# Optimization experiments

Hardware: AMD Instinct MI355X
Metric: run time of the kernel (lower is better)

## Reference

```python
import jax, jax.numpy as jnp
import numpy as np
import math

NEG = -1e32
B, S, D, H, DFF, L = 16, 512, 1024, 8, 4096, 3
DK = D // H


def layernorm(x, g, b, eps=1e-5):
    mu = x.mean(-1, keepdims=True)
    var = ((x - mu) ** 2).mean(-1, keepdims=True)
    return (x - mu) / jnp.sqrt(var + eps) * g + b


def gen_dam(alphas, E, bmask):
    # alphas, E: [H, S, 2]; hard gumbel-softmax with straight-through
    Hh, Ss, _ = alphas.shape
    g = -jnp.log(E + 1e-5)
    y_soft = jax.nn.softmax(alphas + g, axis=-1)  # tau = 1
    idx = jnp.argmax(y_soft, axis=-1)
    y_hard = jax.nn.one_hot(idx, 2, dtype=y_soft.dtype)
    m = y_hard - jax.lax.stop_gradient(y_soft) + y_soft
    m = jnp.broadcast_to(m[:, :, 0:1], (Hh, Ss, Ss))
    m = jnp.triu(m)
    m = jnp.rot90(m, 1, axes=(1, 2))
    i = jnp.arange(Ss)[:, None]
    j = jnp.arange(Ss)[None, :]
    src = jnp.clip(j - i, 0, Ss - 1)
    shifted = m[:, jnp.arange(Ss)[:, None], src]  # mask_tri[:, i, j] = m[:, i, j - i]
    mask_tri = jnp.where(j >= i, shifted, 0.0)
    masks = mask_tri + jnp.swapaxes(jnp.triu(mask_tri, 1), 1, 2)
    masks = jnp.triu(masks, bmask)
    return masks


def attention(q, k, v, src_mask, dam, zero_pad, gammas):
    # q,k,v: [B,H,S,dk]; src_mask: [S,S] bool; dam: [H,S,S] bool
    dk = q.shape[-1]
    Ss = q.shape[2]
    scores = jnp.einsum('bhqd,bhkd->bhqk', q, k) / math.sqrt(dk)
    damb = dam[None]          # [1,H,S,S]
    smb = src_mask[None, None]  # [1,1,S,S]
    # NOTE: faithful to the torch code, where the first masked_fill(mask==0)
    # result is overwritten - only dam masks the first softmax.
    sc = jnp.where(damb, scores, NEG)
    sc = jax.nn.softmax(sc, axis=-1)
    sc = sc * smb.astype(sc.dtype) * damb.astype(sc.dtype)
    distcum = jnp.cumsum(sc, axis=-1)
    disttot = jnp.sum(sc, axis=-1, keepdims=True)
    pos = jnp.abs(jnp.arange(Ss)[None, :] - jnp.arange(Ss)[:, None]).astype(scores.dtype)
    dist = jnp.sqrt(jnp.clip((disttot - distcum) * pos[None, None], 0.0, None))
    dist = jax.lax.stop_gradient(dist)
    gamma = -jax.nn.softplus(gammas)[None]  # [1,H,1,1]
    te = jnp.clip(jnp.exp(dist * gamma), 1e-5, 1e5)
    scores = scores * te
    scores = jnp.where(smb, scores, NEG)
    scores = jnp.where(damb, scores, NEG)
    scores = jax.nn.softmax(scores, axis=-1)
    if zero_pad:
        scores = scores.at[:, :, 0, :].set(0.0)
    return jnp.einsum('bhqk,bhkd->bhqd', scores, v)


def transformer_layer(bmask, query, key, values, apply_pos, p):
    Bb, Ss, Dd = query.shape
    Hh = p['gammas'].shape[0]
    dam = gen_dam(p['alphas'], p['E'], bmask) == 0
    src_mask = jnp.triu(jnp.ones((Ss, Ss), jnp.int32), bmask) == 0
    k = (key @ p['kW'].T + p['kb']).reshape(Bb, Ss, Hh, -1).transpose(0, 2, 1, 3)
    q = (query @ p['kW'].T + p['kb']).reshape(Bb, Ss, Hh, -1).transpose(0, 2, 1, 3)  # kq_same
    v = (values @ p['vW'].T + p['vb']).reshape(Bb, Ss, Hh, -1).transpose(0, 2, 1, 3)
    att = attention(q, k, v, src_mask, dam, bmask == 0, p['gammas'])
    concat = att.transpose(0, 2, 1, 3).reshape(Bb, Ss, Dd)
    q2 = concat @ p['oW'].T + p['ob']
    x = layernorm(query + q2, p['ln1_g'], p['ln1_b'])
    if apply_pos:
        ff = jax.nn.relu(x @ p['w1'].T + p['b1']) @ p['w2'].T + p['b2']
        x = layernorm(x + ff, p['ln2_g'], p['ln2_b'])
    return x


def setup_inputs() -> dict:
    key = jax.random.key(0)
    ks = jax.random.split(key, 16)
    sc = 0.02
    return {
        'q_embed_data': jax.random.normal(ks[0], (B, S, D), jnp.float32),
        'qa_embed_data': jax.random.normal(ks[1], (B, S, D), jnp.float32),
        'kW': sc * jax.random.normal(ks[2], (L, D, D), jnp.float32),
        'kb': jnp.zeros((L, D), jnp.float32),
        'vW': sc * jax.random.normal(ks[3], (L, D, D), jnp.float32),
        'vb': jnp.zeros((L, D), jnp.float32),
        'oW': sc * jax.random.normal(ks[4], (L, D, D), jnp.float32),
        'ob': jnp.zeros((L, D), jnp.float32),
        'gammas': 0.5 * jax.random.normal(ks[5], (L, H, 1, 1), jnp.float32),
        'alphas': 0.001 * jax.random.normal(ks[6], (L, H, S, 2), jnp.float32),
        'ln1_g': jnp.ones((L, D), jnp.float32),
        'ln1_b': jnp.zeros((L, D), jnp.float32),
        'w1': sc * jax.random.normal(ks[7], (L, DFF, D), jnp.float32),
        'b1': jnp.zeros((L, DFF), jnp.float32),
        'w2': sc * jax.random.normal(ks[8], (L, D, DFF), jnp.float32),
        'b2': jnp.zeros((L, D), jnp.float32),
        'ln2_g': jnp.ones((L, D), jnp.float32),
        'ln2_b': jnp.zeros((L, D), jnp.float32),
        'gumbel_E': jax.random.exponential(ks[9], (L, H, S, 2), jnp.float32),
    }


def reference(q_embed_data, qa_embed_data, kW, kb, vW, vb, oW, ob, gammas,
              alphas, ln1_g, ln1_b, w1, b1, w2, b2, ln2_g, ln2_b, gumbel_E):
    def P(l):
        return {'kW': kW[l], 'kb': kb[l], 'vW': vW[l], 'vb': vb[l],
                'oW': oW[l], 'ob': ob[l], 'gammas': gammas[l], 'alphas': alphas[l],
                'ln1_g': ln1_g[l], 'ln1_b': ln1_b[l], 'w1': w1[l], 'b1': b1[l],
                'w2': w2[l], 'b2': b2[l], 'ln2_g': ln2_g[l], 'ln2_b': ln2_b[l],
                'E': gumbel_E[l]}
    # blocks_1: self-attention over answer embedding (mask=1)
    y = transformer_layer(1, qa_embed_data, qa_embed_data, qa_embed_data, True, P(0))
    # blocks_2: self-attn on question emb (no FFN), then cross-attn into y
    x = transformer_layer(1, q_embed_data, q_embed_data, q_embed_data, False, P(1))
    x = transformer_layer(0, x, x, y, True, P(2))
    return x
```

## Files before the change

### kernel.cpp

```cpp
#include <hip/hip_runtime.h>
#include <math.h>

#define NEGV -1e32f

typedef __bf16 bf16_t;
typedef _Float16 f16_t;
typedef __bf16 bf16x8 __attribute__((ext_vector_type(8)));
typedef __bf16 bf16x4 __attribute__((ext_vector_type(4)));
typedef _Float16 f16x8 __attribute__((ext_vector_type(8)));
typedef float floatx4 __attribute__((ext_vector_type(4)));

static __device__ __forceinline__ float wave_sum(float v) {
#pragma unroll
  for (int d = 32; d > 0; d >>= 1) v += __shfl_xor(v, d, 64);
  return v;
}
static __device__ __forceinline__ float wave_max(float v) {
#pragma unroll
  for (int d = 32; d > 0; d >>= 1) v = fmaxf(v, __shfl_xor(v, d, 64));
  return v;
}

static __device__ __forceinline__ void gl2lds16(const bf16_t* g, bf16_t* l) {
  __builtin_amdgcn_global_load_lds((__attribute__((address_space(1))) void*)(void*)g,
                                   (__attribute__((address_space(3))) void*)l, 16, 0, 0);
}

template <int BIAS_MODE, bool RELU, int OUT_MODE>
__global__ __launch_bounds__(256) void gemm_bt(
    const bf16_t* __restrict__ A, long lda, long a_so, long a_si,
    const bf16_t* __restrict__ B, long ldb, long b_so, long b_si,
    void* __restrict__ Cv, long ldc, long c_so, long c_si,
    const float* __restrict__ bias, int zdiv, int K, float alpha)
{
  __shared__ bf16_t As[8192];
  __shared__ bf16_t Bs[8192];
  const int tid = threadIdx.x;
  const int wave = tid >> 6;
  const int lane = tid & 63;
  const int wr = wave >> 1;
  const int wc = wave & 1;
  const int z = blockIdx.z;
  const long zo = z / zdiv;
  const long zi = z % zdiv;
  A += zo * a_so + zi * a_si;
  B += zo * b_so + zi * b_si;
  const long m0 = (long)blockIdx.x * 128;
  const long n0 = (long)blockIdx.y * 128;

  const int srow = tid >> 3;
  const int scol = ((tid & 7) ^ (srow & 7)) * 8;
  const bf16_t* gA = A + (m0 + srow) * lda + scol;
  const bf16_t* gB = B + (n0 + srow) * ldb + scol;
  bf16_t* lA = As + wave * 512;
  bf16_t* lB = Bs + wave * 512;

  floatx4 acc[4][4] = {};
  const int lr = lane & 15;
  const int kg = lane >> 4;

  for (int k0 = 0; k0 < K; k0 += 64) {
#pragma unroll
    for (int r = 0; r < 4; ++r) {
      gl2lds16(gA + (long)r * 32 * lda + k0, lA + r * 2048);
      gl2lds16(gB + (long)r * 32 * ldb + k0, lB + r * 2048);
    }
    __syncthreads();
#pragma unroll
    for (int h = 0; h < 2; ++h) {
      const int slot = ((h * 4 + kg) ^ (lr & 7)) * 8;
      bf16x8 af[4], bfr[4];
#pragma unroll
      for (int t = 0; t < 4; ++t) {
        af[t]  = *(const bf16x8*)(As + (wr * 64 + t * 16 + lr) * 64 + slot);
        bfr[t] = *(const bf16x8*)(Bs + (wc * 64 + t * 16 + lr) * 64 + slot);
      }
#pragma unroll
      for (int tm = 0; tm < 4; ++tm)
#pragma unroll
        for (int tn = 0; tn < 4; ++tn)
          acc[tm][tn] = __builtin_amdgcn_mfma_f32_16x16x32_bf16(af[tm], bfr[tn], acc[tm][tn], 0, 0, 0);
    }
    __syncthreads();
  }

  const long coff = zo * c_so + zi * c_si;
  const int q4 = (lane >> 4) * 4;
#pragma unroll
  for (int tm = 0; tm < 4; ++tm) {
#pragma unroll
    for (int tn = 0; tn < 4; ++tn) {
#pragma unroll
      for (int r = 0; r < 4; ++r) {
        const long row = m0 + wr * 64 + tm * 16 + q4 + r;
        const long col = n0 + wc * 64 + tn * 16 + lr;
        float v = acc[tm][tn][r] * alpha;
        if (BIAS_MODE == 1) v += bias[col];
        if (BIAS_MODE == 2) v += bias[row];
        if (RELU) v = fmaxf(v, 0.0f);
        const long idx = coff + row * ldc + col;
        if (OUT_MODE == 1)      ((bf16_t*)Cv)[idx] = (bf16_t)v;
        else if (OUT_MODE == 2) ((f16_t*)Cv)[idx]  = (f16_t)v;
        else                    ((float*)Cv)[idx]  = v;
      }
    }
  }
}

__global__ __launch_bounds__(256) void cast_kernel(const float* __restrict__ in,
                                                   bf16_t* __restrict__ out, long n)
{
  const long i = ((long)blockIdx.x * 256 + threadIdx.x) * 4;
  if (i >= n) return;
  const float4 v = *(const float4*)(in + i);
  bf16x4 o;
  o[0] = (bf16_t)v.x; o[1] = (bf16_t)v.y; o[2] = (bf16_t)v.z; o[3] = (bf16_t)v.w;
  *(bf16x4*)(out + i) = o;
}

__global__ void bbit_kernel(const float* __restrict__ alphas, const float* __restrict__ E,
                            int* __restrict__ bbit, int n)
{
  const int i = blockIdx.x * 256 + threadIdx.x;
  if (i >= n) return;
  const float l0 = alphas[2 * i]     - logf(E[2 * i]     + 1e-5f);
  const float l1 = alphas[2 * i + 1] - logf(E[2 * i + 1] + 1e-5f);
  bbit[i] = (l0 >= l1) ? 1 : 0;
}

template <bool XBF>
__global__ __launch_bounds__(256) void ln_kernel(
    const void* __restrict__ Xv, const float* __restrict__ R,
    const float* __restrict__ g, const float* __restrict__ b,
    float* __restrict__ out32, bf16_t* __restrict__ out16)
{
  const long row = blockIdx.x;
  const int t = threadIdx.x;
  float x0, x1, x2, x3;
  if (XBF) {
    const bf16x4 xv = *(const bf16x4*)((const bf16_t*)Xv + row * 1024 + t * 4);
    x0 = (float)xv[0]; x1 = (float)xv[1]; x2 = (float)xv[2]; x3 = (float)xv[3];
  } else {
    const float4 xv = *(const float4*)((const float*)Xv + row * 1024 + t * 4);
    x0 = xv.x; x1 = xv.y; x2 = xv.z; x3 = xv.w;
  }
  const float4 rv = *(const float4*)(R + row * 1024 + t * 4);
  const float v0 = x0 + rv.x, v1 = x1 + rv.y, v2 = x2 + rv.z, v3 = x3 + rv.w;
  float s  = v0 + v1 + v2 + v3;
  float s2 = v0 * v0 + v1 * v1 + v2 * v2 + v3 * v3;
  s = wave_sum(s); s2 = wave_sum(s2);
  __shared__ float red[8];
  const int wv = t >> 6, lane = t & 63;
  if (lane == 0) { red[wv] = s; red[4 + wv] = s2; }
  __syncthreads();
  s  = red[0] + red[1] + red[2] + red[3];
  s2 = red[4] + red[5] + red[6] + red[7];
  const float mu = s * (1.0f / 1024.0f);
  const float var = s2 * (1.0f / 1024.0f) - mu * mu;
  const float rstd = rsqrtf(var + 1e-5f);
  const float4 gv = *(const float4*)(g + t * 4);
  const float4 bv = *(const float4*)(b + t * 4);
  float4 ov;
  ov.x = (v0 - mu) * rstd * gv.x + bv.x;
  ov.y = (v1 - mu) * rstd * gv.y + bv.y;
  ov.z = (v2 - mu) * rstd * gv.z + bv.z;
  ov.w = (v3 - mu) * rstd * gv.w + bv.w;
  if (out32) *(float4*)(out32 + row * 1024 + t * 4) = ov;
  if (out16) {
    bf16x4 oh;
    oh[0] = (bf16_t)ov.x; oh[1] = (bf16_t)ov.y; oh[2] = (bf16_t)ov.z; oh[3] = (bf16_t)ov.w;
    *(bf16x4*)(out16 + row * 1024 + t * 4) = oh;
  }
}

__global__ __launch_bounds__(256) void attn_mid(
    const f16_t* __restrict__ S, bf16_t* __restrict__ P,
    const int* __restrict__ bbit, const float* __restrict__ gam,
    const int bmask, const int zero_pad)
{
  const int wid = threadIdx.x >> 6;
  const int lane = threadIdx.x & 63;
  const long rowid = (long)blockIdx.x * 4 + wid;
  const int i = (int)(rowid & 511);
  const int h = (int)(rowid >> 9) & 7;
  const f16_t* s = S + rowid * 512;
  const int jb = lane * 8;

  const float gv = gam[h];
  const float gamma = -log1pf(expf(gv));

  float sv[8];
  {
    const f16x8 a = *(const f16x8*)(s + jb);
#pragma unroll
    for (int u = 0; u < 8; ++u) sv[u] = (float)a[u];
  }
  const int* bb = bbit + h * 512;
  float z[8];
  bool band[8];
  float m1 = NEGV;
#pragma unroll
  for (int u = 0; u < 8; ++u) {
    const int j = jb + u;
    const bool bd = j < i + bmask;
    band[u] = bd;
    int d = j - i; d = d < 0 ? 0 : d;
    const bool allowed = bd || (bb[d] == 0);
    z[u] = allowed ? sv[u] : NEGV;
    m1 = fmaxf(m1, z[u]);
  }
  m1 = wave_max(m1);
  float e[8], es = 0.f;
#pragma unroll
  for (int u = 0; u < 8; ++u) { e[u] = expf(z[u] - m1); es += e[u]; }
  es = wave_sum(es);
  const float inv1 = 1.0f / es;

  float c[8];
  float run = 0.f;
#pragma unroll
  for (int u = 0; u < 8; ++u) {
    const float p = band[u] ? e[u] * inv1 : 0.f;
    run += p;
    c[u] = run;
  }
  float x = run;
#pragma unroll
  for (int d = 1; d < 64; d <<= 1) {
    const float y = __shfl_up(x, (unsigned)d, 64);
    if (lane >= d) x += y;
  }
  const float tot = __shfl(x, 63, 64);
  const float ex = x - run;

  float z2[8];
  float m2 = NEGV;
#pragma unroll
  for (int u = 0; u < 8; ++u) {
    const int j = jb + u;
    const float cc = c[u] + ex;
    const float pos = fabsf((float)(i - j));
    const float dist = sqrtf(fmaxf((tot - cc) * pos, 0.f));
    float te = expf(dist * gamma);
    te = fminf(fmaxf(te, 1e-5f), 1e5f);
    z2[u] = band[u] ? sv[u] * te : NEGV;
    m2 = fmaxf(m2, z2[u]);
  }
  m2 = wave_max(m2);
  float f[8], es2 = 0.f;
#pragma unroll
  for (int u = 0; u < 8; ++u) { f[u] = expf(z2[u] - m2); es2 += f[u]; }
  es2 = wave_sum(es2);
  const float inv2 = (zero_pad && i == 0) ? 0.f : (1.0f / es2);
  bf16x8 o;
#pragma unroll
  for (int u = 0; u < 8; ++u) o[u] = (bf16_t)(f[u] * inv2);
  *(bf16x8*)(P + rowid * 512 + jb) = o;
}

extern "C" void kernel_launch(void* const* d_in, const int* in_sizes, int n_in,
                              void* d_out, int out_size, void* d_ws, size_t ws_size,
                              hipStream_t stream)
{
  (void)in_sizes; (void)n_in; (void)out_size; (void)ws_size;
  const float* q_emb  = (const float*)d_in[0];
  const float* qa_emb = (const float*)d_in[1];
  const float* kW = (const float*)d_in[2];
  const float* kb = (const float*)d_in[3];
  const float* vW = (const float*)d_in[4];
  const float* vb = (const float*)d_in[5];
  const float* oW = (const float*)d_in[6];
  const float* ob = (const float*)d_in[7];
  const float* gammas = (const float*)d_in[8];
  const float* alphas = (const float*)d_in[9];
  const float* ln1_g = (const float*)d_in[10];
  const float* ln1_b = (const float*)d_in[11];
  const float* w1 = (const float*)d_in[12];
  const float* b1 = (const float*)d_in[13];
  const float* w2 = (const float*)d_in[14];
  const float* b2 = (const float*)d_in[15];
  const float* ln2_g = (const float*)d_in[16];
  const float* ln2_b = (const float*)d_in[17];
  const float* gumE = (const float*)d_in[18];
  float* outp = (float*)d_out;

  const size_t MBc = 1ull << 20;
  char* W = (char*)d_ws;
  int*    bbit = (int*)W;
  bf16_t* VB   = (bf16_t*)(W + 1 * MBc);
  bf16_t* XB   = (bf16_t*)(W + 17 * MBc);
  bf16_t* kWb  = (bf16_t*)(W + 33 * MBc);
  bf16_t* vWb  = (bf16_t*)(W + 39 * MBc);
  bf16_t* oWb  = (bf16_t*)(W + 45 * MBc);
  bf16_t* w1b  = (bf16_t*)(W + 51 * MBc);
  bf16_t* w2b  = (bf16_t*)(W + 59 * MBc);
  bf16_t* KQB  = (bf16_t*)(W + 67 * MBc);
  bf16_t* VT   = (bf16_t*)(W + 83 * MBc);
  f16_t*  SSPP = (f16_t*)(W + 99 * MBc);
  bf16_t* PPb  = (bf16_t*)(W + 99 * MBc);
  bf16_t* ATT  = (bf16_t*)(W + 163 * MBc);
  float*  O32  = (float*)(W + 67 * MBc);
  bf16_t* X1B  = (bf16_t*)(W + 99 * MBc);
  bf16_t* H1B  = (bf16_t*)(W + 115 * MBc);

  const long ND = 8388608;

  auto run_layer = [&](int l, const void* Qin, bool qin_bf16, const bf16_t* XBp,
                       const bf16_t* VBp, bool apply_pos, int bmask,
                       float* o32, bf16_t* o16) {
    const bf16_t* kWl = kWb + (long)l * 1048576;
    const bf16_t* vWl = vWb + (long)l * 1048576;
    const bf16_t* oWl = oWb + (long)l * 1048576;
    gemm_bt<1, false, 1><<<dim3(64, 8, 1), dim3(256), 0, stream>>>(
        XBp, 1024, 0, 0, kWl, 1024, 0, 0, (void*)KQB, 1024, 0, 0,
        kb + l * 1024, 1, 1024, 1.0f);
    gemm_bt<2, false, 1><<<dim3(8, 4, 16), dim3(256), 0, stream>>>(
        vWl, 1024, 0, 0, VBp, 1024, 524288, 0, (void*)VT, 512, 524288, 0,
        vb + l * 1024, 1, 1024, 1.0f);
    const int zp = (bmask == 0) ? 1 : 0;
    gemm_bt<0, false, 2><<<dim3(4, 4, 128), dim3(256), 0, stream>>>(
        KQB, 1024, 524288, 128, KQB, 1024, 524288, 128,
        (void*)SSPP, 512, 2097152, 262144, nullptr, 8, 128, 0.08838834764831845f);
    attn_mid<<<dim3(16384), dim3(256), 0, stream>>>(
        SSPP, PPb, bbit + l * 4096, gammas + l * 8, bmask, zp);
    gemm_bt<0, false, 1><<<dim3(4, 1, 128), dim3(256), 0, stream>>>(
        PPb, 512, 2097152, 262144, VT, 512, 524288, 65536,
        (void*)ATT, 1024, 524288, 128, nullptr, 8, 512, 1.0f);
    gemm_bt<1, false, 0><<<dim3(64, 8, 1), dim3(256), 0, stream>>>(
        ATT, 1024, 0, 0, oWl, 1024, 0, 0, (void*)O32, 1024, 0, 0,
        ob + l * 1024, 1, 1024, 1.0f);
    if (!apply_pos) {
      if (qin_bf16)
        ln_kernel<true><<<dim3(8192), dim3(256), 0, stream>>>(
            Qin, O32, ln1_g + l * 1024, ln1_b + l * 1024, o32, o16);
      else
        ln_kernel<false><<<dim3(8192), dim3(256), 0, stream>>>(
            Qin, O32, ln1_g + l * 1024, ln1_b + l * 1024, o32, o16);
    } else {
      cast_kernel<<<dim3(4096), dim3(256), 0, stream>>>(w1 + (long)l * 4194304, w1b, 4194304);
      cast_kernel<<<dim3(4096), dim3(256), 0, stream>>>(w2 + (long)l * 4194304, w2b, 4194304);
      if (qin_bf16)
        ln_kernel<true><<<dim3(8192), dim3(256), 0, stream>>>(
            Qin, O32, ln1_g + l * 1024, ln1_b + l * 1024, nullptr, X1B);
      else
        ln_kernel<false><<<dim3(8192), dim3(256), 0, stream>>>(
            Qin, O32, ln1_g + l * 1024, ln1_b + l * 1024, nullptr, X1B);
      gemm_bt<1, true, 1><<<dim3(64, 32, 1), dim3(256), 0, stream>>>(
          X1B, 1024, 0, 0, w1b, 1024, 0, 0, (void*)H1B, 4096, 0, 0,
          b1 + l * 4096, 1, 1024, 1.0f);
      gemm_bt<1, false, 0><<<dim3(64, 8, 1), dim3(256), 0, stream>>>(
          H1B, 4096, 0, 0, w2b, 4096, 0, 0, (void*)O32, 1024, 0, 0,
          b2 + l * 1024, 1, 4096, 1.0f);
      ln_kernel<true><<<dim3(8192), dim3(256), 0, stream>>>(
          X1B, O32, ln2_g + l * 1024, ln2_b + l * 1024, o32, o16);
    }
  };

  bbit_kernel<<<dim3(48), dim3(256), 0, stream>>>(alphas, gumE, bbit, 12288);
  cast_kernel<<<dim3(3072), dim3(256), 0, stream>>>(kW, kWb, 3145728);
  cast_kernel<<<dim3(3072), dim3(256), 0, stream>>>(vW, vWb, 3145728);
  cast_kernel<<<dim3(3072), dim3(256), 0, stream>>>(oW, oWb, 3145728);

  cast_kernel<<<dim3(8192), dim3(256), 0, stream>>>(qa_emb, XB, ND);
  run_layer(0, qa_emb, false, XB, XB, true, 1, nullptr, VB);
  cast_kernel<<<dim3(8192), dim3(256), 0, stream>>>(q_emb, XB, ND);
  run_layer(1, q_emb, false, XB, XB, false, 1, nullptr, XB);
  run_layer(2, XB, true, XB, VB, true, 0, outp, nullptr);
}
```

Baseline: 1.282 ms.

## Add double-buffered LDS GEMM and use larger tiles for FFN1

Adds a templated GEMM kernel that double-buffers LDS tiles, issuing the direct global-to-LDS loads for the next K-slab while MFMAs run on the current one. All projection, PV and FFN GEMMs except the QK score GEMM switch to it. FFN1 also moves to a larger 256x256 tile with 512 threads and 128KB of dynamic LDS. The aim is to hide global load latency and improve data reuse, at the cost of more LDS per block and therefore lower occupancy.

```diff
diff --git a/kernel.cpp b/kernel.cpp
--- a/kernel.cpp
+++ b/kernel.cpp
@@ -24,6 +24,118 @@
 static __device__ __forceinline__ void gl2lds16(const bf16_t* g, bf16_t* l) {
   __builtin_amdgcn_global_load_lds((__attribute__((address_space(1))) void*)(void*)g,
                                    (__attribute__((address_space(3))) void*)l, 16, 0, 0);
+}
+
+template <int WM, int WN, int FM, int FN, int BIAS_MODE, bool RELU, int OUT_MODE>
+__global__ __launch_bounds__(WM * WN * 64) void gemm_db(
+    const bf16_t* __restrict__ A, long lda, long a_so, long a_si,
+    const bf16_t* __restrict__ B, long ldb, long b_so, long b_si,
+    void* __restrict__ Cv, long ldc, long c_so, long c_si,
+    const float* __restrict__ bias, int zdiv, int K, float alpha)
+{
+  constexpr int THREADS = WM * WN * 64;
+  constexpr int BM = WM * FM * 16;
+  constexpr int BN = WN * FN * 16;
+  constexpr int RR = THREADS / 8;
+  constexpr int RA = BM / RR;
+  constexpr int RB = BN / RR;
+  constexpr int NSTG = RA + RB;
+  extern __shared__ bf16_t smem[];
+  bf16_t* const Asb = smem;
+  bf16_t* const Bsb = smem + 2 * (BM * 64);
+
+  const int tid = threadIdx.x;
+  const int wave = tid >> 6;
+  const int lane = tid & 63;
+  const int wm = wave / WN;
+  const int wn = wave % WN;
+  const int z = blockIdx.z;
+  const long zo = z / zdiv;
+  const long zi = z % zdiv;
+  A += zo * a_so + zi * a_si;
+  B += zo * b_so + zi * b_si;
+  const long m0 = (long)blockIdx.x * BM;
+  const long n0 = (long)blockIdx.y * BN;
+
+  const int srow = tid >> 3;
+  const int scol = ((tid & 7) ^ (srow & 7)) * 8;
+  const bf16_t* gA = A + (m0 + srow) * lda + scol;
+  const bf16_t* gB = B + (n0 + srow) * ldb + scol;
+  const int lofs = wave * 512;
+
+  floatx4 acc[FM][FN] = {};
+  const int lr = lane & 15;
+  const int kg = lane >> 4;
+  const int NT = K >> 6;
+
+  {
+    bf16_t* lA = Asb + lofs;
+    bf16_t* lB = Bsb + lofs;
+#pragma unroll
+    for (int r = 0; r < RA; ++r) gl2lds16(gA + (long)(r * RR) * lda, lA + r * RR * 64);
+#pragma unroll
+    for (int r = 0; r < RB; ++r) gl2lds16(gB + (long)(r * RR) * ldb, lB + r * RR * 64);
+  }
+
+  for (int t = 0; t < NT; ++t) {
+    const int buf = t & 1;
+    if (t + 1 < NT) {
+      const long ko = (long)(t + 1) * 64;
+      bf16_t* lA = Asb + (buf ^ 1) * (BM * 64) + lofs;
+      bf16_t* lB = Bsb + (buf ^ 1) * (BN * 64) + lofs;
+#pragma unroll
+      for (int r = 0; r < RA; ++r) gl2lds16(gA + (long)(r * RR) * lda + ko, lA + r * RR * 64);
+#pragma unroll
+      for (int r = 0; r < RB; ++r) gl2lds16(gB + (long)(r * RR) * ldb + ko, lB + r * RR * 64);
+      asm volatile("s_waitcnt vmcnt(%0)" :: "n"(NSTG) : "memory");
+    } else {
+      asm volatile("s_waitcnt vmcnt(0)" ::: "memory");
+    }
+    __builtin_amdgcn_s_barrier();
+    __builtin_amdgcn_sched_barrier(0);
+    const bf16_t* __restrict__ Ab = Asb + buf * (BM * 64);
+    const bf16_t* __restrict__ Bb = Bsb + buf * (BN * 64);
+#pragma unroll
+    for (int h = 0; h < 2; ++h) {
+      const int slot = ((h * 4 + kg) ^ (lr & 7)) * 8;
+      bf16x8 af[FM], bfr[FN];
+#pragma unroll
+      for (int m = 0; m < FM; ++m)
+        af[m] = *(const bf16x8*)(Ab + (wm * (FM * 16) + m * 16 + lr) * 64 + slot);
+#pragma unroll
+      for (int n = 0; n < FN; ++n)
+        bfr[n] = *(const bf16x8*)(Bb + (wn * (FN * 16) + n * 16 + lr) * 64 + slot);
+#pragma unroll
+      for (int m = 0; m < FM; ++m)
+#pragma unroll
+        for (int n = 0; n < FN; ++n)
+          acc[m][n] = __builtin_amdgcn_mfma_f32_16x16x32_bf16(af[m], bfr[n], acc[m][n], 0, 0, 0);
+    }
+    __builtin_amdgcn_sched_barrier(0);
+    __builtin_amdgcn_s_barrier();
+  }
+
+  const long coff = zo * c_so + zi * c_si;
+  const int q4 = (lane >> 4) * 4;
+#pragma unroll
+  for (int m = 0; m < FM; ++m) {
+#pragma unroll
+    for (int n = 0; n < FN; ++n) {
+#pragma unroll
+      for (int r = 0; r < 4; ++r) {
+        const long row = m0 + wm * (FM * 16) + m * 16 + q4 + r;
+        const long col = n0 + wn * (FN * 16) + n * 16 + lr;
+        float v = acc[m][n][r] * alpha;
+        if (BIAS_MODE == 1) v += bias[col];
+        if (BIAS_MODE == 2) v += bias[row];
+        if (RELU) v = fmaxf(v, 0.0f);
+        const long idx = coff + row * ldc + col;
+        if (OUT_MODE == 1)      ((bf16_t*)Cv)[idx] = (bf16_t)v;
+        else if (OUT_MODE == 2) ((f16_t*)Cv)[idx]  = (f16_t)v;
+        else                    ((float*)Cv)[idx]  = v;
+      }
+    }
+  }
 }
 
 template <int BIAS_MODE, bool RELU, int OUT_MODE>
@@ -284,6 +396,21 @@
   const float* gumE = (const float*)d_in[18];
   float* outp = (float*)d_out;
 
+  static bool attr_done = false;
+  if (!attr_done) {
+    attr_done = true;
+    (void)hipFuncSetAttribute(reinterpret_cast<const void*>(&gemm_db<2,2,4,4,1,false,1>),
+                              hipFuncAttributeMaxDynamicSharedMemorySize, 65536);
+    (void)hipFuncSetAttribute(reinterpret_cast<const void*>(&gemm_db<2,2,4,4,2,false,1>),
+                              hipFuncAttributeMaxDynamicSharedMemorySize, 65536);
+    (void)hipFuncSetAttribute(reinterpret_cast<const void*>(&gemm_db<2,2,4,4,0,false,1>),
+                              hipFuncAttributeMaxDynamicSharedMemorySize, 65536);
+    (void)hipFuncSetAttribute(reinterpret_cast<const void*>(&gemm_db<2,2,4,4,1,false,0>),
+                              hipFuncAttributeMaxDynamicSharedMemorySize, 65536);
+    (void)hipFuncSetAttribute(reinterpret_cast<const void*>(&gemm_db<2,4,8,4,1,true,1>),
+                              hipFuncAttributeMaxDynamicSharedMemorySize, 131072);
+  }
+
   const size_t MBc = 1ull << 20;
   char* W = (char*)d_ws;
   int*    bbit = (int*)W;
@@ -311,10 +438,10 @@
     const bf16_t* kWl = kWb + (long)l * 1048576;
     const bf16_t* vWl = vWb + (long)l * 1048576;
     const bf16_t* oWl = oWb + (long)l * 1048576;
-    gemm_bt<1, false, 1><<<dim3(64, 8, 1), dim3(256), 0, stream>>>(
+    gemm_db<2,2,4,4,1,false,1><<<dim3(64, 8, 1), dim3(256), 65536, stream>>>(
         XBp, 1024, 0, 0, kWl, 1024, 0, 0, (void*)KQB, 1024, 0, 0,
         kb + l * 1024, 1, 1024, 1.0f);
-    gemm_bt<2, false, 1><<<dim3(8, 4, 16), dim3(256), 0, stream>>>(
+    gemm_db<2,2,4,4,2,false,1><<<dim3(8, 4, 16), dim3(256), 65536, stream>>>(
         vWl, 1024, 0, 0, VBp, 1024, 524288, 0, (void*)VT, 512, 524288, 0,
         vb + l * 1024, 1, 1024, 1.0f);
     const int zp = (bmask == 0) ? 1 : 0;
@@ -323,10 +450,10 @@
         (void*)SSPP, 512, 2097152, 262144, nullptr, 8, 128, 0.08838834764831845f);
     attn_mid<<<dim3(16384), dim3(256), 0, stream>>>(
         SSPP, PPb, bbit + l * 4096, gammas + l * 8, bmask, zp);
-    gemm_bt<0, false, 1><<<dim3(4, 1, 128), dim3(256), 0, stream>>>(
+    gemm_db<2,2,4,4,0,false,1><<<dim3(4, 1, 128), dim3(256), 65536, stream>>>(
         PPb, 512, 2097152, 262144, VT, 512, 524288, 65536,
         (void*)ATT, 1024, 524288, 128, nullptr, 8, 512, 1.0f);
-    gemm_bt<1, false, 0><<<dim3(64, 8, 1), dim3(256), 0, stream>>>(
+    gemm_db<2,2,4,4,1,false,0><<<dim3(64, 8, 1), dim3(256), 65536, stream>>>(
         ATT, 1024, 0, 0, oWl, 1024, 0, 0, (void*)O32, 1024, 0, 0,
         ob + l * 1024, 1, 1024, 1.0f);
     if (!apply_pos) {
@@ -345,10 +472,10 @@
       else
         ln_kernel<false><<<dim3(8192), dim3(256), 0, stream>>>(
             Qin, O32, ln1_g + l * 1024, ln1_b + l * 1024, nullptr, X1B);
-      gemm_bt<1, true, 1><<<dim3(64, 32, 1), dim3(256), 0, stream>>>(
+      gemm_db<2,4,8,4,1,true,1><<<dim3(32, 16, 1), dim3(512), 131072, stream>>>(
           X1B, 1024, 0, 0, w1b, 1024, 0, 0, (void*)H1B, 4096, 0, 0,
           b1 + l * 4096, 1, 1024, 1.0f);
-      gemm_bt<1, false, 0><<<dim3(64, 8, 1), dim3(256), 0, stream>>>(
+      gemm_db<2,2,4,4,1,false,0><<<dim3(64, 8, 1), dim3(256), 65536, stream>>>(
           H1B, 4096, 0, 0, w2b, 4096, 0, 0, (void*)O32, 1024, 0, 0,
           b2 + l * 1024, 1, 4096, 1.0f);
       ln_kernel<true><<<dim3(8192), dim3(256), 0, stream>>>(
```

Result: faster. 1.169 ms (-8.9%).
